# Kernel tuning notes

Measured on AMD Instinct MI355X. Metric: run time of the kernel, lower is better.

The kernel has to match this reference:

```python
import jax, jax.numpy as jnp
import numpy as np

COMMITMENT_COST = 0.25


def setup_inputs() -> dict:
    key = jax.random.key(0)
    k1, k2 = jax.random.split(key)
    x = jax.random.normal(k1, (64, 32, 32, 64), dtype=jnp.float32)
    # VarianceScaling default: scale=1.0, fan_in truncated-normal-ish; plain scaled normal is fine for a reference
    embeddings = jax.random.normal(k2, (1024, 64), dtype=jnp.float32) * (1.0 / np.sqrt(64))
    return {"x": x, "embeddings": embeddings}


def reference(x, embeddings):
    K, D = embeddings.shape
    flat = x.reshape(-1, D)  # [N, D]
    distances = (
        jnp.sum(flat * flat, axis=1, keepdims=True)
        - 2.0 * (flat @ embeddings.T)
        + jnp.sum(embeddings * embeddings, axis=1)
    )
    encoding_indices = jnp.argmin(distances, axis=1)  # [N]
    # one-hot @ embeddings is just a gather
    quantized = embeddings[encoding_indices].reshape(x.shape)

    e_latent_loss = jnp.mean((jax.lax.stop_gradient(quantized) - x) ** 2)
    q_latent_loss = jnp.mean((quantized - jax.lax.stop_gradient(x)) ** 2)
    loss = q_latent_loss + COMMITMENT_COST * e_latent_loss

    # straight-through estimator
    quantized_st = x + jax.lax.stop_gradient(quantized - x)
    return quantized_st, loss
```

## Files before the change

### kernel.cpp

```cpp
#include <hip/hip_runtime.h>

#define DIM   64
#define NROWS 65536
#define NCODE 1024
#define RPB   64
#define NBLK  (NROWS / RPB)

typedef float    f32x4 __attribute__((ext_vector_type(4)));
typedef _Float16 f16x8 __attribute__((ext_vector_type(8)));

union U4H { uint4 u; f16x8 h; };

__device__ __forceinline__ void split2(float f, unsigned short& hb,
                                       unsigned short& lb) {
  _Float16 h = (_Float16)f;
  float r = f - (float)h;
  _Float16 lo = (_Float16)r;
  hb = __builtin_bit_cast(unsigned short, h);
  lb = __builtin_bit_cast(unsigned short, lo);
}
__device__ __forceinline__ uint4 pack8(const unsigned short* p) {
  return make_uint4((unsigned)p[0] | ((unsigned)p[1] << 16),
                    (unsigned)p[2] | ((unsigned)p[3] << 16),
                    (unsigned)p[4] | ((unsigned)p[5] << 16),
                    (unsigned)p[6] | ((unsigned)p[7] << 16));
}

__global__ __launch_bounds__(256) void vq_esplit(const float* __restrict__ e,
                                                 unsigned short* __restrict__ eB,
                                                 float* __restrict__ e2h,
                                                 float* __restrict__ loss) {
  const int c = blockIdx.x * 256 + threadIdx.x;
  if (c == 0) *loss = 0.f;
  const int gt = c >> 4, cl = c & 15;
  float s = 0.f;
  #pragma unroll
  for (int kh = 0; kh < 2; ++kh) {
    #pragma unroll
    for (int g = 0; g < 4; ++g) {
      const float* ep = e + (size_t)c * DIM + kh * 32 + g * 8;
      float4 v0 = *(const float4*)ep;
      float4 v1 = *(const float4*)(ep + 4);
      float f[8] = {v0.x, v0.y, v0.z, v0.w, v1.x, v1.y, v1.z, v1.w};
      unsigned short hb[8], lb[8];
      #pragma unroll
      for (int j = 0; j < 8; ++j) {
        split2(f[j], hb[j], lb[j]);
        s = fmaf(f[j], f[j], s);
      }
      const size_t pos = (size_t)((g << 4) | cl) * 8;
      const size_t tb = (size_t)gt * 2048;
      *(uint4*)(eB + tb + (kh * 2 + 0) * 512 + pos) = pack8(hb);
      *(uint4*)(eB + tb + (kh * 2 + 1) * 512 + pos) = pack8(lb);
    }
  }
  e2h[c] = 0.5f * s;
}

__device__ __forceinline__ void load_lds16(const void* gsrc, void* ldst) {
  __builtin_amdgcn_global_load_lds(
      (const __attribute__((address_space(1))) unsigned int*)
          (unsigned long long)gsrc,
      (__attribute__((address_space(3))) unsigned int*)
          (unsigned long long)ldst,
      16, 0, 0);
}

__global__ __launch_bounds__(256, 2) void vq_main(
    const float* __restrict__ x,
    const float* __restrict__ e,
    const unsigned short* __restrict__ eB,
    const float* __restrict__ e2h,
    float* __restrict__ out,
    float* __restrict__ loss)
{
  __shared__ __align__(16) unsigned short tiles[8 * 2048];
  __shared__ __align__(16) float e2L[NCODE];
  __shared__ int   kFin[RPB];
  __shared__ float lossP[4];

  const int t   = threadIdx.x;
  const int l   = t & 63;
  const int wv  = t >> 6;
  const int col = l & 15;
  const int g   = l >> 4;
  const int B0  = blockIdx.x * RPB;
  const int R0  = B0 + wv * 16;
  const int ph  = (blockIdx.x * 23) & 63;

  float4 xv[4];
  #pragma unroll
  for (int kh = 0; kh < 2; ++kh) {
    const float* xp = x + (size_t)(R0 + col) * DIM + kh * 32 + g * 8;
    xv[kh * 2 + 0] = *(const float4*)xp;
    xv[kh * 2 + 1] = *(const float4*)(xp + 4);
  }

#define STAGE(CTL)                                                        \
  do {                                                                    \
    const int pt_ = (ph + (CTL)) & 63;                                    \
    load_lds16(eB + (size_t)pt_ * 2048 + wv * 512 + (size_t)l * 8,        \
               tiles + ((CTL) & 7) * 2048 + wv * 512);                    \
  } while (0)

  load_lds16(e2h + wv * 256 + l * 4, e2L + wv * 256);
  STAGE(0); STAGE(1); STAGE(2); STAGE(3); STAGE(4); STAGE(5);

  f16x8 a[2][2];
  float x2p = 0.f;
  #pragma unroll
  for (int kh = 0; kh < 2; ++kh) {
    float4 v0 = xv[kh * 2], v1 = xv[kh * 2 + 1];
    float f[8] = {v0.x, v0.y, v0.z, v0.w, v1.x, v1.y, v1.z, v1.w};
    unsigned short hb[8], lb[8];
    #pragma unroll
    for (int j = 0; j < 8; ++j) {
      split2(f[j], hb[j], lb[j]);
      x2p = fmaf(f[j], f[j], x2p);
    }
    U4H uh; uh.u = pack8(hb); a[kh][0] = uh.h;
    U4H ul; ul.u = pack8(lb); a[kh][1] = ul.h;
  }
  #pragma unroll
  for (int off = 1; off < 64; off <<= 1) x2p += __shfl_xor(x2p, off, 64);

  float bestS[4];
  int   bestK[4];
  #pragma unroll
  for (int r = 0; r < 4; ++r) { bestS[r] = -3.402823466e38f; bestK[r] = 0x7FFFFFFF; }

#define VMWAIT(N)                                              \
  do {                                                         \
    asm volatile("s_waitcnt vmcnt(" #N ")" ::: "memory");      \
    __builtin_amdgcn_sched_barrier(0);                         \
  } while (0)

  #pragma unroll 8
  for (int m = 0; m < 64; ++m) {
    VMWAIT(5);
    __builtin_amdgcn_s_barrier();
    STAGE(m + 6);
    {
      const int pt = (ph + m) & 63;
      const unsigned short* sl = tiles + (m & 7) * 2048;
      uint4 u0 = *(const uint4*)(sl + 0 * 512 + l * 8);
      uint4 u1 = *(const uint4*)(sl + 1 * 512 + l * 8);
      uint4 u2 = *(const uint4*)(sl + 2 * 512 + l * 8);
      uint4 u3 = *(const uint4*)(sl + 3 * 512 + l * 8);
      const float ne2 = -e2L[pt * 16 + col];
      U4H q0, q1, q2, q3; q0.u = u0; q1.u = u1; q2.u = u2; q3.u = u3;
      const int kk0 = pt * 16 + col;
      f32x4 c0 = {ne2, ne2, ne2, ne2};
      f32x4 c1 = {0.f, 0.f, 0.f, 0.f};
      c0 = __builtin_amdgcn_mfma_f32_16x16x32_f16(a[0][0], q0.h, c0, 0, 0, 0);
      c1 = __builtin_amdgcn_mfma_f32_16x16x32_f16(a[1][0], q2.h, c1, 0, 0, 0);
      c0 = __builtin_amdgcn_mfma_f32_16x16x32_f16(a[0][1], q0.h, c0, 0, 0, 0);
      c1 = __builtin_amdgcn_mfma_f32_16x16x32_f16(a[1][1], q2.h, c1, 0, 0, 0);
      c0 = __builtin_amdgcn_mfma_f32_16x16x32_f16(a[0][0], q1.h, c0, 0, 0, 0);
      c1 = __builtin_amdgcn_mfma_f32_16x16x32_f16(a[1][0], q3.h, c1, 0, 0, 0);
      #pragma unroll
      for (int r = 0; r < 4; ++r) {
        float sv = c0[r] + c1[r];
        bool take = (sv > bestS[r]) || (sv == bestS[r] && kk0 < bestK[r]);
        if (take) { bestS[r] = sv; bestK[r] = kk0; }
      }
    }
  }

  #pragma unroll
  for (int off = 1; off <= 8; off <<= 1) {
    #pragma unroll
    for (int r = 0; r < 4; ++r) {
      float sp = __shfl_xor(bestS[r], off, 64);
      int   kp = __shfl_xor(bestK[r], off, 64);
      if (sp > bestS[r] || (sp == bestS[r] && kp < bestK[r])) {
        bestS[r] = sp; bestK[r] = kp;
      }
    }
  }

  float ssum = 0.f;
  if (col == 0) {
    #pragma unroll
    for (int r = 0; r < 4; ++r) {
      kFin[wv * 16 + g * 4 + r] = bestK[r];
      ssum += bestS[r];
    }
  }
  ssum += __shfl_xor(ssum, 16, 64);
  ssum += __shfl_xor(ssum, 32, 64);
  if (l == 0)
    lossP[wv] = fmaf(-2.f, ssum, x2p);

  __syncthreads();
  if (t == 0) {
    float bl = (lossP[0] + lossP[1]) + (lossP[2] + lossP[3]);
    atomicAdd(loss, bl * (1.25f / (float)((size_t)NROWS * DIM)));
  }

  {
    const int row = t >> 2, seg = t & 3;
    const int bk = kFin[row];
    const float4* src = (const float4*)(e + (size_t)bk * DIM + seg * 16);
    float4* dst = (float4*)(out + (size_t)(B0 + row) * DIM + seg * 16);
    #pragma unroll
    for (int i = 0; i < 4; ++i) dst[i] = src[i];
  }
}

extern "C" void kernel_launch(void* const* d_in, const int* in_sizes, int n_in,
                              void* d_out, int out_size, void* d_ws, size_t ws_size,
                              hipStream_t stream) {
  const float* x = (const float*)d_in[0];
  const float* e = (const float*)d_in[1];
  float* out  = (float*)d_out;
  float* loss = out + (size_t)NROWS * DIM;

  unsigned short* eB = (unsigned short*)d_ws;
  float* e2h = (float*)((char*)d_ws + 64 * 2048 * 2);

  vq_esplit<<<NCODE / 256, 256, 0, stream>>>(e, eB, e2h, loss);
  vq_main  <<<NBLK, 256, 0, stream>>>(x, e, eB, e2h, out, loss);
}
```

Measured before the change: 49.12 us.

## Keep codebook slices in registers and stream x tiles through LDS

Swaps the dataflow. Before, each 256-thread block held 64 rows of x in registers and streamed the whole fp16-split codebook through LDS. Now each 1024-thread block has 16 waves, and each wave keeps a fixed 64-code slice of the codebook in registers. Blocks of 16 rows of x are double-buffered through LDS, and per-wave argmin partials are merged in LDS at the end. The aim is to cut the repeated codebook traffic from global memory into LDS and the per-step barriers. In exchange the kernel uses many more registers (launch bounds 1024,4), launches only 256 blocks, adds a block-wide barrier per batch, and has a more complex cross-wave reduction.

```diff
diff --git a/kernel.cpp b/kernel.cpp
--- a/kernel.cpp
+++ b/kernel.cpp
@@ -3,7 +3,7 @@
 #define DIM   64
 #define NROWS 65536
 #define NCODE 1024
-#define RPB   64
+#define RPB   256
 #define NBLK  (NROWS / RPB)
 
 typedef float    f32x4 __attribute__((ext_vector_type(4)));
@@ -66,7 +66,7 @@
       16, 0, 0);
 }
 
-__global__ __launch_bounds__(256, 2) void vq_main(
+__global__ __launch_bounds__(1024, 4) void vq_main(
     const float* __restrict__ x,
     const float* __restrict__ e,
     const unsigned short* __restrict__ eB,
@@ -74,10 +74,11 @@
     float* __restrict__ out,
     float* __restrict__ loss)
 {
-  __shared__ __align__(16) unsigned short tiles[8 * 2048];
-  __shared__ __align__(16) float e2L[NCODE];
+  __shared__ __align__(16) float xbuf[2][1024];
+  __shared__ float bestSL[16][RPB];
+  __shared__ int   bestKL[16][RPB];
   __shared__ int   kFin[RPB];
-  __shared__ float lossP[4];
+  __shared__ float lossW[17];
 
   const int t   = threadIdx.x;
   const int l   = t & 63;
@@ -85,126 +86,149 @@
   const int col = l & 15;
   const int g   = l >> 4;
   const int B0  = blockIdx.x * RPB;
-  const int R0  = B0 + wv * 16;
-  const int ph  = (blockIdx.x * 23) & 63;
-
-  float4 xv[4];
+
+  uint4 bfr[16];
+  {
+    const unsigned short* ebw = eB + (size_t)(wv * 4) * 2048 + (size_t)l * 8;
+    #pragma unroll
+    for (int ct = 0; ct < 4; ++ct)
+      #pragma unroll
+      for (int q = 0; q < 4; ++q)
+        bfr[ct * 4 + q] = *(const uint4*)(ebw + ct * 2048 + q * 512);
+  }
+  float e2v[4];
   #pragma unroll
-  for (int kh = 0; kh < 2; ++kh) {
-    const float* xp = x + (size_t)(R0 + col) * DIM + kh * 32 + g * 8;
-    xv[kh * 2 + 0] = *(const float4*)xp;
-    xv[kh * 2 + 1] = *(const float4*)(xp + 4);
-  }
-
-#define STAGE(CTL)                                                        \
-  do {                                                                    \
-    const int pt_ = (ph + (CTL)) & 63;                                    \
-    load_lds16(eB + (size_t)pt_ * 2048 + wv * 512 + (size_t)l * 8,        \
-               tiles + ((CTL) & 7) * 2048 + wv * 512);                    \
+  for (int ct = 0; ct < 4; ++ct) e2v[ct] = e2h[wv * 64 + ct * 16 + col];
+
+  const float* xsrc = x + (size_t)(B0 + col) * DIM + (wv >> 1) * 32 + g * 8 + (wv & 1) * 4;
+
+#define XSTAGE(M, B)                                                     \
+  do { if (wv < 4)                                                       \
+    load_lds16(xsrc + (size_t)(M) * (16 * DIM),                          \
+               &xbuf[B][0] + wv * 256 + l * 4);                          \
   } while (0)
 
-  load_lds16(e2h + wv * 256 + l * 4, e2L + wv * 256);
-  STAGE(0); STAGE(1); STAGE(2); STAGE(3); STAGE(4); STAGE(5);
-
-  f16x8 a[2][2];
-  float x2p = 0.f;
-  #pragma unroll
-  for (int kh = 0; kh < 2; ++kh) {
-    float4 v0 = xv[kh * 2], v1 = xv[kh * 2 + 1];
-    float f[8] = {v0.x, v0.y, v0.z, v0.w, v1.x, v1.y, v1.z, v1.w};
-    unsigned short hb[8], lb[8];
-    #pragma unroll
-    for (int j = 0; j < 8; ++j) {
-      split2(f[j], hb[j], lb[j]);
-      x2p = fmaf(f[j], f[j], x2p);
+  XSTAGE(0, 0);
+  asm volatile("s_waitcnt vmcnt(0)" ::: "memory");
+  __builtin_amdgcn_s_barrier();
+  __builtin_amdgcn_sched_barrier(0);
+
+  float x2acc = 0.f;
+
+#define BATCH(M, RB)                                                          \
+  do {                                                                        \
+    if ((M) < 15) XSTAGE((M) + 1, 1 - (RB));                                  \
+    const float* xb = &xbuf[RB][0] + g * 64 + col * 4;                        \
+    float4 x00 = *(const float4*)(xb + 0);                                    \
+    float4 x01 = *(const float4*)(xb + 256);                                  \
+    float4 x10 = *(const float4*)(xb + 512);                                  \
+    float4 x11 = *(const float4*)(xb + 768);                                  \
+    float xf[16] = {x00.x, x00.y, x00.z, x00.w, x01.x, x01.y, x01.z, x01.w,   \
+                    x10.x, x10.y, x10.z, x10.w, x11.x, x11.y, x11.z, x11.w};  \
+    unsigned short hb[16], lb[16];                                            \
+    _Pragma("unroll")                                                         \
+    for (int j = 0; j < 16; ++j) split2(xf[j], hb[j], lb[j]);                 \
+    if (wv == 0) {                                                            \
+      _Pragma("unroll")                                                       \
+      for (int j = 0; j < 16; ++j) x2acc = fmaf(xf[j], xf[j], x2acc);         \
+    }                                                                         \
+    U4H ah0, ah1, al0, al1;                                                   \
+    ah0.u = pack8(hb); ah1.u = pack8(hb + 8);                                 \
+    al0.u = pack8(lb); al1.u = pack8(lb + 8);                                 \
+    float bS[4]; int bK[4];                                                   \
+    _Pragma("unroll")                                                         \
+    for (int r = 0; r < 4; ++r) { bS[r] = -3.402823466e38f; bK[r] = 0; }      \
+    _Pragma("unroll")                                                         \
+    for (int ct = 0; ct < 4; ++ct) {                                          \
+      U4H q0, q1, q2, q3;                                                     \
+      q0.u = bfr[ct * 4 + 0]; q1.u = bfr[ct * 4 + 1];                         \
+      q2.u = bfr[ct * 4 + 2]; q3.u = bfr[ct * 4 + 3];                         \
+      const float ne2 = -e2v[ct];                                             \
+      f32x4 c0 = {ne2, ne2, ne2, ne2};                                        \
+      f32x4 c1 = {0.f, 0.f, 0.f, 0.f};                                        \
+      c0 = __builtin_amdgcn_mfma_f32_16x16x32_f16(ah0.h, q0.h, c0, 0, 0, 0);  \
+      c1 = __builtin_amdgcn_mfma_f32_16x16x32_f16(ah1.h, q2.h, c1, 0, 0, 0);  \
+      c0 = __builtin_amdgcn_mfma_f32_16x16x32_f16(al0.h, q0.h, c0, 0, 0, 0);  \
+      c1 = __builtin_amdgcn_mfma_f32_16x16x32_f16(al1.h, q2.h, c1, 0, 0, 0);  \
+      c0 = __builtin_amdgcn_mfma_f32_16x16x32_f16(ah0.h, q1.h, c0, 0, 0, 0);  \
+      c1 = __builtin_amdgcn_mfma_f32_16x16x32_f16(ah1.h, q3.h, c1, 0, 0, 0);  \
+      const int kk = wv * 64 + ct * 16 + col;                                 \
+      _Pragma("unroll")                                                       \
+      for (int r = 0; r < 4; ++r) {                                           \
+        float sv = c0[r] + c1[r];                                             \
+        if (sv > bS[r]) { bS[r] = sv; bK[r] = kk; }                           \
+      }                                                                       \
+    }                                                                         \
+    _Pragma("unroll")                                                         \
+    for (int off = 1; off <= 8; off <<= 1) {                                  \
+      _Pragma("unroll")                                                       \
+      for (int r = 0; r < 4; ++r) {                                           \
+        float sp = __shfl_xor(bS[r], off, 64);                                \
+        int   kp = __shfl_xor(bK[r], off, 64);                                \
+        if (sp > bS[r] || (sp == bS[r] && kp < bK[r])) {                      \
+          bS[r] = sp; bK[r] = kp;                                             \
+        }                                                                     \
+      }                                                                       \
+    }                                                                         \
+    if (col == 0) {                                                           \
+      _Pragma("unroll")                                                       \
+      for (int r = 0; r < 4; ++r) {                                           \
+        bestSL[wv][(M) * 16 + g * 4 + r] = bS[r];                             \
+        bestKL[wv][(M) * 16 + g * 4 + r] = bK[r];                             \
+      }                                                                       \
+    }                                                                         \
+    asm volatile("s_waitcnt vmcnt(0)" ::: "memory");                          \
+    __builtin_amdgcn_s_barrier();                                             \
+    __builtin_amdgcn_sched_barrier(0);                                        \
+  } while (0)
+
+  #pragma unroll 1
+  for (int mm = 0; mm < 8; ++mm) {
+    BATCH(2 * mm + 0, 0);
+    BATCH(2 * mm + 1, 1);
+  }
+
+  {
+    const int row = t >> 2, q = t & 3;
+    float s = bestSL[q * 4 + 0][row]; int k = bestKL[q * 4 + 0][row];
+    #pragma unroll
+    for (int j = 1; j < 4; ++j) {
+      float s2 = bestSL[q * 4 + j][row]; int k2 = bestKL[q * 4 + j][row];
+      if (s2 > s || (s2 == s && k2 < k)) { s = s2; k = k2; }
     }
-    U4H uh; uh.u = pack8(hb); a[kh][0] = uh.h;
-    U4H ul; ul.u = pack8(lb); a[kh][1] = ul.h;
-  }
-  #pragma unroll
-  for (int off = 1; off < 64; off <<= 1) x2p += __shfl_xor(x2p, off, 64);
-
-  float bestS[4];
-  int   bestK[4];
-  #pragma unroll
-  for (int r = 0; r < 4; ++r) { bestS[r] = -3.402823466e38f; bestK[r] = 0x7FFFFFFF; }
-
-#define VMWAIT(N)                                              \
-  do {                                                         \
-    asm volatile("s_waitcnt vmcnt(" #N ")" ::: "memory");      \
-    __builtin_amdgcn_sched_barrier(0);                         \
-  } while (0)
-
-  #pragma unroll 8
-  for (int m = 0; m < 64; ++m) {
-    VMWAIT(5);
-    __builtin_amdgcn_s_barrier();
-    STAGE(m + 6);
-    {
-      const int pt = (ph + m) & 63;
-      const unsigned short* sl = tiles + (m & 7) * 2048;
-      uint4 u0 = *(const uint4*)(sl + 0 * 512 + l * 8);
-      uint4 u1 = *(const uint4*)(sl + 1 * 512 + l * 8);
-      uint4 u2 = *(const uint4*)(sl + 2 * 512 + l * 8);
-      uint4 u3 = *(const uint4*)(sl + 3 * 512 + l * 8);
-      const float ne2 = -e2L[pt * 16 + col];
-      U4H q0, q1, q2, q3; q0.u = u0; q1.u = u1; q2.u = u2; q3.u = u3;
-      const int kk0 = pt * 16 + col;
-      f32x4 c0 = {ne2, ne2, ne2, ne2};
-      f32x4 c1 = {0.f, 0.f, 0.f, 0.f};
-      c0 = __builtin_amdgcn_mfma_f32_16x16x32_f16(a[0][0], q0.h, c0, 0, 0, 0);
-      c1 = __builtin_amdgcn_mfma_f32_16x16x32_f16(a[1][0], q2.h, c1, 0, 0, 0);
-      c0 = __builtin_amdgcn_mfma_f32_16x16x32_f16(a[0][1], q0.h, c0, 0, 0, 0);
-      c1 = __builtin_amdgcn_mfma_f32_16x16x32_f16(a[1][1], q2.h, c1, 0, 0, 0);
-      c0 = __builtin_amdgcn_mfma_f32_16x16x32_f16(a[0][0], q1.h, c0, 0, 0, 0);
-      c1 = __builtin_amdgcn_mfma_f32_16x16x32_f16(a[1][0], q3.h, c1, 0, 0, 0);
-      #pragma unroll
-      for (int r = 0; r < 4; ++r) {
-        float sv = c0[r] + c1[r];
-        bool take = (sv > bestS[r]) || (sv == bestS[r] && kk0 < bestK[r]);
-        if (take) { bestS[r] = sv; bestK[r] = kk0; }
-      }
+    #pragma unroll
+    for (int off = 1; off <= 2; off <<= 1) {
+      float s2 = __shfl_xor(s, off, 64);
+      int   k2 = __shfl_xor(k, off, 64);
+      if (s2 > s || (s2 == s && k2 < k)) { s = s2; k = k2; }
     }
-  }
-
-  #pragma unroll
-  for (int off = 1; off <= 8; off <<= 1) {
-    #pragma unroll
-    for (int r = 0; r < 4; ++r) {
-      float sp = __shfl_xor(bestS[r], off, 64);
-      int   kp = __shfl_xor(bestK[r], off, 64);
-      if (sp > bestS[r] || (sp == bestS[r] && kp < bestK[r])) {
-        bestS[r] = sp; bestK[r] = kp;
-      }
-    }
-  }
-
-  float ssum = 0.f;
-  if (col == 0) {
-    #pragma unroll
-    for (int r = 0; r < 4; ++r) {
-      kFin[wv * 16 + g * 4 + r] = bestK[r];
-      ssum += bestS[r];
-    }
-  }
-  ssum += __shfl_xor(ssum, 16, 64);
-  ssum += __shfl_xor(ssum, 32, 64);
-  if (l == 0)
-    lossP[wv] = fmaf(-2.f, ssum, x2p);
-
+    if (q == 0) kFin[row] = k;
+    float sc = (q == 0) ? s : 0.f;
+    #pragma unroll
+    for (int off = 1; off < 64; off <<= 1) sc += __shfl_xor(sc, off, 64);
+    if (l == 0) lossW[wv] = sc;
+  }
+  if (wv == 0) {
+    float xs = x2acc;
+    #pragma unroll
+    for (int off = 1; off < 64; off <<= 1) xs += __shfl_xor(xs, off, 64);
+    if (l == 0) lossW[16] = xs;
+  }
   __syncthreads();
   if (t == 0) {
-    float bl = (lossP[0] + lossP[1]) + (lossP[2] + lossP[3]);
-    atomicAdd(loss, bl * (1.25f / (float)((size_t)NROWS * DIM)));
-  }
-
-  {
-    const int row = t >> 2, seg = t & 3;
-    const int bk = kFin[row];
-    const float4* src = (const float4*)(e + (size_t)bk * DIM + seg * 16);
-    float4* dst = (float4*)(out + (size_t)(B0 + row) * DIM + seg * 16);
-    #pragma unroll
-    for (int i = 0; i < 4; ++i) dst[i] = src[i];
+    float ss = 0.f;
+    #pragma unroll
+    for (int i = 0; i < 16; ++i) ss += lossW[i];
+    atomicAdd(loss, fmaf(-2.f, ss, lossW[16]) * (1.25f / (float)((size_t)NROWS * DIM)));
+  }
+
+  #pragma unroll
+  for (int i = 0; i < 4; ++i) {
+    const int id  = t + i * 1024;
+    const int row = id >> 4, seg = id & 15;
+    const int bk  = kFin[row];
+    *(float4*)(out + (size_t)(B0 + row) * DIM + seg * 4) =
+        *(const float4*)(e + (size_t)bk * DIM + seg * 4);
   }
 }
 
@@ -220,5 +244,5 @@
   float* e2h = (float*)((char*)d_ws + 64 * 2048 * 2);
 
   vq_esplit<<<NCODE / 256, 256, 0, stream>>>(e, eB, e2h, loss);
-  vq_main  <<<NBLK, 256, 0, stream>>>(x, e, eB, e2h, out, loss);
-}
+  vq_main  <<<NBLK, 1024, 0, stream>>>(x, e, eB, e2h, out, loss);
+}
```

Result: slower. 93.89 us (+91.1%).

## Double block size and stage codebook in 4-tile groups through 3-slot ring

Applied to the files above, without the earlier changes.

The main kernel now runs 512 threads (8 waves) per block covering 128 rows, halving the grid. Each wave helps copy a group of four codebook tiles into a three-slot LDS ring. Each barrier is followed by four tile MFMA passes instead of one, so there are a quarter as many barriers per block. The trade-offs are lower prefetch depth, a non-unrolled outer loop, a larger per-block LDS footprint, and the e2h preload now reading past the 1024 valid entries into workspace.

```diff
diff --git a/kernel.cpp b/kernel.cpp
--- a/kernel.cpp
+++ b/kernel.cpp
@@ -3,7 +3,7 @@
 #define DIM   64
 #define NROWS 65536
 #define NCODE 1024
-#define RPB   64
+#define RPB   128
 #define NBLK  (NROWS / RPB)
 
 typedef float    f32x4 __attribute__((ext_vector_type(4)));
@@ -66,7 +66,7 @@
       16, 0, 0);
 }
 
-__global__ __launch_bounds__(256, 2) void vq_main(
+__global__ __launch_bounds__(512) void vq_main(
     const float* __restrict__ x,
     const float* __restrict__ e,
     const unsigned short* __restrict__ eB,
@@ -74,10 +74,10 @@
     float* __restrict__ out,
     float* __restrict__ loss)
 {
-  __shared__ __align__(16) unsigned short tiles[8 * 2048];
-  __shared__ __align__(16) float e2L[NCODE];
+  __shared__ __align__(16) unsigned short ring[3][4 * 2048];
+  __shared__ __align__(16) float e2L[2048];
   __shared__ int   kFin[RPB];
-  __shared__ float lossP[4];
+  __shared__ float lossP[8];
 
   const int t   = threadIdx.x;
   const int l   = t & 63;
@@ -86,7 +86,7 @@
   const int g   = l >> 4;
   const int B0  = blockIdx.x * RPB;
   const int R0  = B0 + wv * 16;
-  const int ph  = (blockIdx.x * 23) & 63;
+  const int pg  = (blockIdx.x * 5) & 15;
 
   float4 xv[4];
   #pragma unroll
@@ -96,15 +96,20 @@
     xv[kh * 2 + 1] = *(const float4*)(xp + 4);
   }
 
-#define STAGE(CTL)                                                        \
-  do {                                                                    \
-    const int pt_ = (ph + (CTL)) & 63;                                    \
-    load_lds16(eB + (size_t)pt_ * 2048 + wv * 512 + (size_t)l * 8,        \
-               tiles + ((CTL) & 7) * 2048 + wv * 512);                    \
+#define STAGEG(GIDX, SLOT)                                                    \
+  do {                                                                        \
+    const int gs_ = (pg + (GIDX)) & 15;                                       \
+    const unsigned short* src_ = eB +                                         \
+        ((size_t)gs_ * 4 + (wv >> 1)) * 2048 + (wv & 1) * 1024 + (size_t)l * 8; \
+    unsigned short* dst_ =                                                    \
+        &ring[SLOT][0] + (wv >> 1) * 2048 + (wv & 1) * 1024;                  \
+    load_lds16(src_, dst_);                                                   \
+    load_lds16(src_ + 512, dst_ + 512);                                       \
   } while (0)
 
   load_lds16(e2h + wv * 256 + l * 4, e2L + wv * 256);
-  STAGE(0); STAGE(1); STAGE(2); STAGE(3); STAGE(4); STAGE(5);
+  STAGEG(0, 0);
+  STAGEG(1, 1);
 
   f16x8 a[2][2];
   float x2p = 0.f;
@@ -129,27 +134,31 @@
   #pragma unroll
   for (int r = 0; r < 4; ++r) { bestS[r] = -3.402823466e38f; bestK[r] = 0x7FFFFFFF; }
 
-#define VMWAIT(N)                                              \
+#define VMWAIT2                                                \
   do {                                                         \
-    asm volatile("s_waitcnt vmcnt(" #N ")" ::: "memory");      \
+    asm volatile("s_waitcnt vmcnt(2)" ::: "memory");           \
     __builtin_amdgcn_sched_barrier(0);                         \
   } while (0)
 
-  #pragma unroll 8
-  for (int m = 0; m < 64; ++m) {
-    VMWAIT(5);
+  int sCur = 0, sStg = 2;
+  #pragma unroll 1
+  for (int m = 0; m < 16; ++m) {
+    VMWAIT2;
     __builtin_amdgcn_s_barrier();
-    STAGE(m + 6);
-    {
-      const int pt = (ph + m) & 63;
-      const unsigned short* sl = tiles + (m & 7) * 2048;
+    STAGEG(m + 2, sStg);
+    const int gi = (pg + m) & 15;
+    const unsigned short* gb = &ring[sCur][0];
+    #pragma unroll
+    for (int j = 0; j < 4; ++j) {
+      const int tj  = gi * 4 + j;
+      const int kk0 = tj * 16 + col;
+      const unsigned short* sl = gb + j * 2048;
       uint4 u0 = *(const uint4*)(sl + 0 * 512 + l * 8);
       uint4 u1 = *(const uint4*)(sl + 1 * 512 + l * 8);
       uint4 u2 = *(const uint4*)(sl + 2 * 512 + l * 8);
       uint4 u3 = *(const uint4*)(sl + 3 * 512 + l * 8);
-      const float ne2 = -e2L[pt * 16 + col];
+      const float ne2 = -e2L[kk0];
       U4H q0, q1, q2, q3; q0.u = u0; q1.u = u1; q2.u = u2; q3.u = u3;
-      const int kk0 = pt * 16 + col;
       f32x4 c0 = {ne2, ne2, ne2, ne2};
       f32x4 c1 = {0.f, 0.f, 0.f, 0.f};
       c0 = __builtin_amdgcn_mfma_f32_16x16x32_f16(a[0][0], q0.h, c0, 0, 0, 0);
@@ -165,6 +174,8 @@
         if (take) { bestS[r] = sv; bestK[r] = kk0; }
       }
     }
+    sCur = (sCur == 2) ? 0 : sCur + 1;
+    sStg = (sStg == 2) ? 0 : sStg + 1;
   }
 
   #pragma unroll
@@ -194,7 +205,8 @@
 
   __syncthreads();
   if (t == 0) {
-    float bl = (lossP[0] + lossP[1]) + (lossP[2] + lossP[3]);
+    float bl = ((lossP[0] + lossP[1]) + (lossP[2] + lossP[3])) +
+               ((lossP[4] + lossP[5]) + (lossP[6] + lossP[7]));
     atomicAdd(loss, bl * (1.25f / (float)((size_t)NROWS * DIM)));
   }
 
@@ -220,5 +232,5 @@
   float* e2h = (float*)((char*)d_ws + 64 * 2048 * 2);
 
   vq_esplit<<<NCODE / 256, 256, 0, stream>>>(e, eB, e2h, loss);
-  vq_main  <<<NBLK, 256, 0, stream>>>(x, e, eB, e2h, out, loss);
-}
+  vq_main  <<<NBLK, 512, 0, stream>>>(x, e, eB, e2h, out, loss);
+}
```

Result: faster. 47.82 us (-2.6%).

## Split codebook scan across two wave halves and merge argmin in LDS

Applied to the files above, without the earlier changes.

Blocks grow to 512 threads. Two groups of four waves each scan half of the codebook tiles over 32 iterations instead of one group scanning all 64. Each half keeps its own 4-slot LDS ring with 3 tiles in flight. Per-row best scores and indices are merged through shared memory before the loss reduction and the gather write. This shortens the serial per-block loop and raises waves per block, at the cost of an extra LDS merge, a second barrier and a tighter register budget from the new launch bounds.

```diff
diff --git a/kernel.cpp b/kernel.cpp
--- a/kernel.cpp
+++ b/kernel.cpp
@@ -66,7 +66,7 @@
       16, 0, 0);
 }
 
-__global__ __launch_bounds__(256, 2) void vq_main(
+__global__ __launch_bounds__(512, 8) void vq_main(
     const float* __restrict__ x,
     const float* __restrict__ e,
     const unsigned short* __restrict__ eB,
@@ -74,19 +74,23 @@
     float* __restrict__ out,
     float* __restrict__ loss)
 {
-  __shared__ __align__(16) unsigned short tiles[8 * 2048];
+  __shared__ __align__(16) unsigned short ring[2][4][2048];
   __shared__ __align__(16) float e2L[NCODE];
+  __shared__ float bestL[8][16];
+  __shared__ int   kL[8][16];
   __shared__ int   kFin[RPB];
-  __shared__ float lossP[4];
+  __shared__ float x2P[4];
 
   const int t   = threadIdx.x;
   const int l   = t & 63;
   const int wv  = t >> 6;
+  const int h   = wv >> 2;
+  const int rg  = wv & 3;
   const int col = l & 15;
   const int g   = l >> 4;
   const int B0  = blockIdx.x * RPB;
-  const int R0  = B0 + wv * 16;
-  const int ph  = (blockIdx.x * 23) & 63;
+  const int R0  = B0 + rg * 16;
+  const int ph  = (blockIdx.x * 7) & 31;
 
   float4 xv[4];
   #pragma unroll
@@ -96,15 +100,16 @@
     xv[kh * 2 + 1] = *(const float4*)(xp + 4);
   }
 
-#define STAGE(CTL)                                                        \
-  do {                                                                    \
-    const int pt_ = (ph + (CTL)) & 63;                                    \
-    load_lds16(eB + (size_t)pt_ * 2048 + wv * 512 + (size_t)l * 8,        \
-               tiles + ((CTL) & 7) * 2048 + wv * 512);                    \
+  load_lds16(e2h + rg * 256 + l * 4, e2L + rg * 256);
+
+#define STAGE(M)                                                         \
+  do {                                                                   \
+    const int pt_ = h * 32 + ((ph + (M)) & 31);                          \
+    load_lds16(eB + (size_t)pt_ * 2048 + rg * 512 + (size_t)l * 8,       \
+               &ring[h][(M) & 3][0] + rg * 512);                         \
   } while (0)
 
-  load_lds16(e2h + wv * 256 + l * 4, e2L + wv * 256);
-  STAGE(0); STAGE(1); STAGE(2); STAGE(3); STAGE(4); STAGE(5);
+  STAGE(0); STAGE(1); STAGE(2);
 
   f16x8 a[2][2];
   float x2p = 0.f;
@@ -129,41 +134,39 @@
   #pragma unroll
   for (int r = 0; r < 4; ++r) { bestS[r] = -3.402823466e38f; bestK[r] = 0x7FFFFFFF; }
 
-#define VMWAIT(N)                                              \
+#define VMWAIT2                                                \
   do {                                                         \
-    asm volatile("s_waitcnt vmcnt(" #N ")" ::: "memory");      \
+    asm volatile("s_waitcnt vmcnt(2)" ::: "memory");           \
     __builtin_amdgcn_sched_barrier(0);                         \
   } while (0)
 
-  #pragma unroll 8
-  for (int m = 0; m < 64; ++m) {
-    VMWAIT(5);
+  #pragma unroll 4
+  for (int m = 0; m < 32; ++m) {
+    VMWAIT2;
     __builtin_amdgcn_s_barrier();
-    STAGE(m + 6);
-    {
-      const int pt = (ph + m) & 63;
-      const unsigned short* sl = tiles + (m & 7) * 2048;
-      uint4 u0 = *(const uint4*)(sl + 0 * 512 + l * 8);
-      uint4 u1 = *(const uint4*)(sl + 1 * 512 + l * 8);
-      uint4 u2 = *(const uint4*)(sl + 2 * 512 + l * 8);
-      uint4 u3 = *(const uint4*)(sl + 3 * 512 + l * 8);
-      const float ne2 = -e2L[pt * 16 + col];
-      U4H q0, q1, q2, q3; q0.u = u0; q1.u = u1; q2.u = u2; q3.u = u3;
-      const int kk0 = pt * 16 + col;
-      f32x4 c0 = {ne2, ne2, ne2, ne2};
-      f32x4 c1 = {0.f, 0.f, 0.f, 0.f};
-      c0 = __builtin_amdgcn_mfma_f32_16x16x32_f16(a[0][0], q0.h, c0, 0, 0, 0);
-      c1 = __builtin_amdgcn_mfma_f32_16x16x32_f16(a[1][0], q2.h, c1, 0, 0, 0);
-      c0 = __builtin_amdgcn_mfma_f32_16x16x32_f16(a[0][1], q0.h, c0, 0, 0, 0);
-      c1 = __builtin_amdgcn_mfma_f32_16x16x32_f16(a[1][1], q2.h, c1, 0, 0, 0);
-      c0 = __builtin_amdgcn_mfma_f32_16x16x32_f16(a[0][0], q1.h, c0, 0, 0, 0);
-      c1 = __builtin_amdgcn_mfma_f32_16x16x32_f16(a[1][0], q3.h, c1, 0, 0, 0);
-      #pragma unroll
-      for (int r = 0; r < 4; ++r) {
-        float sv = c0[r] + c1[r];
-        bool take = (sv > bestS[r]) || (sv == bestS[r] && kk0 < bestK[r]);
-        if (take) { bestS[r] = sv; bestK[r] = kk0; }
-      }
+    STAGE(m + 3);
+    const int ht  = h * 32 + ((ph + m) & 31);
+    const int kk0 = ht * 16 + col;
+    const unsigned short* sl = &ring[h][m & 3][0];
+    uint4 u0 = *(const uint4*)(sl + 0 * 512 + l * 8);
+    uint4 u1 = *(const uint4*)(sl + 1 * 512 + l * 8);
+    uint4 u2 = *(const uint4*)(sl + 2 * 512 + l * 8);
+    uint4 u3 = *(const uint4*)(sl + 3 * 512 + l * 8);
+    const float ne2 = -e2L[kk0];
+    U4H q0, q1, q2, q3; q0.u = u0; q1.u = u1; q2.u = u2; q3.u = u3;
+    f32x4 c0 = {ne2, ne2, ne2, ne2};
+    f32x4 c1 = {0.f, 0.f, 0.f, 0.f};
+    c0 = __builtin_amdgcn_mfma_f32_16x16x32_f16(a[0][0], q0.h, c0, 0, 0, 0);
+    c1 = __builtin_amdgcn_mfma_f32_16x16x32_f16(a[1][0], q2.h, c1, 0, 0, 0);
+    c0 = __builtin_amdgcn_mfma_f32_16x16x32_f16(a[0][1], q0.h, c0, 0, 0, 0);
+    c1 = __builtin_amdgcn_mfma_f32_16x16x32_f16(a[1][1], q2.h, c1, 0, 0, 0);
+    c0 = __builtin_amdgcn_mfma_f32_16x16x32_f16(a[0][0], q1.h, c0, 0, 0, 0);
+    c1 = __builtin_amdgcn_mfma_f32_16x16x32_f16(a[1][0], q3.h, c1, 0, 0, 0);
+    #pragma unroll
+    for (int r = 0; r < 4; ++r) {
+      float sv = c0[r] + c1[r];
+      bool take = (sv > bestS[r]) || (sv == bestS[r] && kk0 < bestK[r]);
+      if (take) { bestS[r] = sv; bestK[r] = kk0; }
     }
   }
 
@@ -179,32 +182,39 @@
     }
   }
 
-  float ssum = 0.f;
   if (col == 0) {
     #pragma unroll
     for (int r = 0; r < 4; ++r) {
-      kFin[wv * 16 + g * 4 + r] = bestK[r];
-      ssum += bestS[r];
-    }
-  }
-  ssum += __shfl_xor(ssum, 16, 64);
-  ssum += __shfl_xor(ssum, 32, 64);
-  if (l == 0)
-    lossP[wv] = fmaf(-2.f, ssum, x2p);
-
+      bestL[wv][g * 4 + r] = bestS[r];
+      kL[wv][g * 4 + r]    = bestK[r];
+    }
+  }
+  if (h == 0 && l == 0) x2P[rg] = x2p;
   __syncthreads();
-  if (t == 0) {
-    float bl = (lossP[0] + lossP[1]) + (lossP[2] + lossP[3]);
-    atomicAdd(loss, bl * (1.25f / (float)((size_t)NROWS * DIM)));
-  }
+
+  if (t < RPB) {
+    const int rq = t >> 4, ri = t & 15;
+    float s0 = bestL[rq][ri];     int k0 = kL[rq][ri];
+    float s1 = bestL[4 + rq][ri]; int k1 = kL[4 + rq][ri];
+    if (s1 > s0) { s0 = s1; k0 = k1; }
+    kFin[t] = k0;
+    float v = s0;
+    #pragma unroll
+    for (int off = 1; off < 64; off <<= 1) v += __shfl_xor(v, off, 64);
+    if (t == 0) {
+      float x2tot = (x2P[0] + x2P[1]) + (x2P[2] + x2P[3]);
+      atomicAdd(loss, fmaf(-2.f, v, x2tot) * (1.25f / (float)((size_t)NROWS * DIM)));
+    }
+  }
+  __syncthreads();
 
   {
-    const int row = t >> 2, seg = t & 3;
+    const int row = t >> 3, seg = t & 7;
     const int bk = kFin[row];
-    const float4* src = (const float4*)(e + (size_t)bk * DIM + seg * 16);
-    float4* dst = (float4*)(out + (size_t)(B0 + row) * DIM + seg * 16);
-    #pragma unroll
-    for (int i = 0; i < 4; ++i) dst[i] = src[i];
+    const float4* src = (const float4*)(e + (size_t)bk * DIM + seg * 8);
+    float4* dst = (float4*)(out + (size_t)(B0 + row) * DIM + seg * 8);
+    dst[0] = src[0];
+    dst[1] = src[1];
   }
 }
 
@@ -220,5 +230,5 @@
   float* e2h = (float*)((char*)d_ws + 64 * 2048 * 2);
 
   vq_esplit<<<NCODE / 256, 256, 0, stream>>>(e, eB, e2h, loss);
-  vq_main  <<<NBLK, 256, 0, stream>>>(x, e, eB, e2h, out, loss);
-}
+  vq_main  <<<NBLK, 512, 0, stream>>>(x, e, eB, e2h, out, loss);
+}
```

Result: no change. 48.58 us (-1.1%).
